# Optimization experiments

Measured on AMD Instinct MI355X. Metric: run time of the kernel, lower is better.

## Reference

```python
import jax, jax.numpy as jnp
import numpy as np

BATCH = 10
HID = 128
OUT = 7
MAX_LEN = 2048


def setup_inputs() -> dict:
    key = jax.random.key(0)
    ks = jax.random.split(key, 10)
    h0 = jax.random.normal(ks[0], (1, BATCH, HID), dtype=jnp.float32)
    c0 = jax.random.normal(ks[1], (1, BATCH, HID), dtype=jnp.float32)
    # target is a sequence of one-hot vectors, shape (MAX_LEN+1, 1, OUT)
    tgt_idx = jax.random.randint(ks[2], (MAX_LEN + 1,), 0, OUT)
    target_onehot = jax.nn.one_hot(tgt_idx, OUT, dtype=jnp.float32)[:, None, :]
    # per-step teacher-forcing coin flips (torch.rand(1) < 0.5 externalized)
    tf_mask = jax.random.bernoulli(ks[3], 0.5, (MAX_LEN,))
    # LSTM parameters, torch gate order [i, f, g, o]; k = 1/sqrt(HID) init scale
    k = 1.0 / np.sqrt(HID)
    W_ih = jax.random.uniform(ks[4], (4 * HID, OUT), minval=-k, maxval=k, dtype=jnp.float32)
    W_hh = jax.random.uniform(ks[5], (4 * HID, HID), minval=-k, maxval=k, dtype=jnp.float32)
    b_ih = jax.random.uniform(ks[6], (4 * HID,), minval=-k, maxval=k, dtype=jnp.float32)
    b_hh = jax.random.uniform(ks[7], (4 * HID,), minval=-k, maxval=k, dtype=jnp.float32)
    W_out = jax.random.uniform(ks[8], (OUT, HID), minval=-k, maxval=k, dtype=jnp.float32)
    b_out = jax.random.uniform(ks[9], (OUT,), minval=-k, maxval=k, dtype=jnp.float32)
    return dict(h0=h0, c0=c0, target_onehot=target_onehot, tf_mask=tf_mask,
                W_ih=W_ih, W_hh=W_hh, b_ih=b_ih, b_hh=b_hh, W_out=W_out, b_out=b_out)


def reference(h0, c0, target_onehot, tf_mask, W_ih, W_hh, b_ih, b_hh, W_out, b_out):
    # initial decoder input: one-hot at last class for all 10 batch items
    x0 = jnp.zeros((BATCH, OUT), jnp.float32).at[:, OUT - 1].set(1.0)
    tgt_next = target_onehot[1:MAX_LEN + 1, 0, :]  # (MAX_LEN, OUT), fed at step i
    bias = b_ih + b_hh

    def step(carry, inp):
        h, c, x = carry            # h,c: (B,HID); x: (B,OUT)
        tf, tgt = inp              # tf: scalar bool; tgt: (OUT,)
        xr = jax.nn.relu(x)
        gates = xr @ W_ih.T + h @ W_hh.T + bias          # (B, 4*HID)
        i_g, f_g, g_g, o_g = jnp.split(gates, 4, axis=-1)
        c2 = jax.nn.sigmoid(f_g) * c + jax.nn.sigmoid(i_g) * jnp.tanh(g_g)
        h2 = jax.nn.sigmoid(o_g) * jnp.tanh(c2)
        logits = h2 @ W_out.T + b_out                    # (B, OUT)
        greedy = jax.nn.one_hot(jnp.argmax(logits, axis=-1), OUT, dtype=jnp.float32)
        nxt = jnp.where(tf, jnp.broadcast_to(tgt, (BATCH, OUT)), greedy)
        return (h2, c2, nxt), logits

    (hT, cT, _), logits = jax.lax.scan(
        step, (h0[0], c0[0], x0), (tf_mask, tgt_next))
    logits = jnp.transpose(logits, (1, 0, 2))            # (B, MAX_LEN, OUT)
    log_probs = jax.nn.log_softmax(logits, axis=-1)
    return log_probs, (hT[None], cT[None])
```

## Files before the change

### kernel.cpp

```cpp
#include <hip/hip_runtime.h>
#include <math.h>

#define BATCH 10
#define HID 128
#define OUT 7
#define MAXLEN 2048
#define NG 512
#define NT 1024
#define RINGD 512
#define OFF_STATE ((size_t)BATCH * MAXLEN * OUT)

typedef float float4v __attribute__((ext_vector_type(4)));

__device__ __forceinline__ float sigm_(float x) { return 1.0f / (1.0f + __expf(-x)); }
__device__ __forceinline__ float tanh_(float x) { return 1.0f - 2.0f / (1.0f + __expf(2.0f * x)); }

__device__ __forceinline__ float grp8_sum(float v) {
    v += __int_as_float(__builtin_amdgcn_update_dpp(0, __float_as_int(v), 0xB1, 0xF, 0xF, true));
    v += __int_as_float(__builtin_amdgcn_update_dpp(0, __float_as_int(v), 0x4E, 0xF, 0xF, true));
    v += __int_as_float(__builtin_amdgcn_update_dpp(0, __float_as_int(v), 0x141, 0xF, 0xF, true));
    return v;
}

__global__
__attribute__((amdgpu_flat_work_group_size(NT, NT), amdgpu_waves_per_eu(4, 4)))
void decoder_rnn_kernel(const float* __restrict__ h0,
                        const float* __restrict__ c0,
                        const float* __restrict__ tonehot,
                        const void*  __restrict__ tf_raw,
                        const float* __restrict__ Wih,
                        const float* __restrict__ Whh,
                        const float* __restrict__ bih,
                        const float* __restrict__ bhh,
                        const float* __restrict__ Wout,
                        const float* __restrict__ bout,
                        float* __restrict__ out)
{
    __shared__ __align__(16) float h_lds[HID];
    __shared__ __align__(16) float gates_lds[NG];
    __shared__ float wih_eff[OUT * NG];
    __shared__ float ring[RINGD][OUT];
    __shared__ unsigned char tgt8[MAXLEN];
    __shared__ unsigned char tf8[MAXLEN];
    __shared__ int tf_byte_mode;

    const int t    = threadIdx.x;
    const int lane = t & 63;
    const int wv   = t >> 6;
    const int ksl  = lane & 7;
    const int grp  = lane >> 3;
    const int b    = blockIdx.x;
    const int gbase = wv * 32 + grp * 4;

    float4v wgt[4][4];
    #pragma unroll
    for (int j = 0; j < 4; j++)
        #pragma unroll
        for (int c = 0; c < 4; c++)
            wgt[j][c] = *(const float4v*)&Whh[(size_t)(gbase + j) * HID + ksl * 16 + c * 4];

    float4v lw[4];
    #pragma unroll
    for (int c = 0; c < 4; c++) { float4v z = {0.f, 0.f, 0.f, 0.f}; lw[c] = z; }
    if (wv < 2 && grp < OUT) {
        #pragma unroll
        for (int c = 0; c < 4; c++)
            lw[c] = *(const float4v*)&Wout[(size_t)grp * HID + ksl * 16 + c * 4];
    }

    float boutr[OUT];
    #pragma unroll
    for (int j = 0; j < OUT; j++) boutr[j] = bout[j];

    for (int idx = t; idx < OUT * NG; idx += NT) {
        int x = idx >> 9, g = idx & (NG - 1);
        wih_eff[idx] = Wih[g * OUT + x] + bih[g] + bhh[g];
    }
    if (t == 0) tf_byte_mode = 0;
    for (int s = t; s < MAXLEN; s += NT) {
        const float* row = tonehot + (size_t)(s + 1) * OUT;
        int idx = 0;
        #pragma unroll
        for (int j = 0; j < OUT; j++) if (row[j] > 0.5f) idx = j;
        tgt8[s] = (unsigned char)idx;
    }
    __syncthreads();
    {
        const unsigned char* tb = (const unsigned char*)tf_raw;
        int mis = 0;
        for (int p = t; p < MAXLEN; p += NT)
            if ((p & 3) && tb[p]) mis = 1;
        if (mis) atomicOr(&tf_byte_mode, 1);
    }
    float c_reg = 0.f, hv = 0.f;
    if (t < HID) {
        hv    = h0[b * HID + t];
        c_reg = c0[b * HID + t];
        h_lds[t] = hv;
    }
    __syncthreads();
    if (tf_byte_mode) {
        const unsigned char* tb = (const unsigned char*)tf_raw;
        for (int s = t; s < MAXLEN; s += NT) tf8[s] = (tb[s] != 0);
    } else {
        const int* ti = (const int*)tf_raw;
        for (int s = t; s < MAXLEN; s += NT) tf8[s] = (ti[s] != 0);
    }
    __syncthreads();

    float* outlp = out + (size_t)b * MAXLEN * OUT;

    for (int s = 0; s < MAXLEN; s++) {
        float4v hc[4];
        #pragma unroll
        for (int c = 0; c < 4; c++)
            hc[c] = *(const float4v*)&h_lds[ksl * 16 + c * 4];

        float a0 = 0.f, a1 = 0.f, a2 = 0.f, a3 = 0.f;
        #pragma unroll
        for (int c = 0; c < 4; c++)
            #pragma unroll
            for (int e = 0; e < 4; e++) {
                const float hval = hc[c][e];
                a0 = fmaf(wgt[0][c][e], hval, a0);
                a1 = fmaf(wgt[1][c][e], hval, a1);
                a2 = fmaf(wgt[2][c][e], hval, a2);
                a3 = fmaf(wgt[3][c][e], hval, a3);
            }
        float al = 0.f;
        if (wv < 2) {
            #pragma unroll
            for (int c = 0; c < 4; c++)
                #pragma unroll
                for (int e = 0; e < 4; e++)
                    al = fmaf(lw[c][e], hc[c][e], al);
            al = grp8_sum(al);
        }
        a0 = grp8_sum(a0);
        a1 = grp8_sum(a1);
        a2 = grp8_sum(a2);
        a3 = grp8_sum(a3);
        if (ksl == 0) {
            float4v g4;
            g4[0] = a0; g4[1] = a1; g4[2] = a2; g4[3] = a3;
            *(float4v*)&gates_lds[gbase] = g4;
        }
        __syncthreads();

        if (t < HID) {
            int xsel = OUT - 1;
            if (s > 0) {
                float lg[OUT];
                lg[0] = __int_as_float(__builtin_amdgcn_readlane(__float_as_int(al),  0)) + boutr[0];
                lg[1] = __int_as_float(__builtin_amdgcn_readlane(__float_as_int(al),  8)) + boutr[1];
                lg[2] = __int_as_float(__builtin_amdgcn_readlane(__float_as_int(al), 16)) + boutr[2];
                lg[3] = __int_as_float(__builtin_amdgcn_readlane(__float_as_int(al), 24)) + boutr[3];
                lg[4] = __int_as_float(__builtin_amdgcn_readlane(__float_as_int(al), 32)) + boutr[4];
                lg[5] = __int_as_float(__builtin_amdgcn_readlane(__float_as_int(al), 40)) + boutr[5];
                lg[6] = __int_as_float(__builtin_amdgcn_readlane(__float_as_int(al), 48)) + boutr[6];
                float bv = lg[0]; int bi = 0;
                #pragma unroll
                for (int j = 1; j < OUT; j++) if (lg[j] > bv) { bv = lg[j]; bi = j; }
                xsel = tf8[s - 1] ? (int)tgt8[s - 1] : bi;
                if (wv == 0 && ksl == 0 && grp < OUT)
                    ring[(s - 1) & (RINGD - 1)][grp] = al;
            }
            const int xo = xsel * NG;
            float ri = gates_lds[t]           + wih_eff[xo + t];
            float rf = gates_lds[HID + t]     + wih_eff[xo + HID + t];
            float rg = gates_lds[2 * HID + t] + wih_eff[xo + 2 * HID + t];
            float ro = gates_lds[3 * HID + t] + wih_eff[xo + 3 * HID + t];
            float cn = sigm_(rf) * c_reg + sigm_(ri) * tanh_(rg);
            c_reg = cn;
            hv = sigm_(ro) * tanh_(cn);
            h_lds[t] = hv;
        } else if (t >= 512 && t < 768 && (s & 255) == 1 && s > 256) {
            const int step = (s - 257) + (t - 512);
            const int slot = step & (RINGD - 1);
            float v[OUT];
            #pragma unroll
            for (int j = 0; j < OUT; j++) v[j] = ring[slot][j] + boutr[j];
            float mx = v[0];
            #pragma unroll
            for (int j = 1; j < OUT; j++) mx = fmaxf(mx, v[j]);
            float sum = 0.f;
            #pragma unroll
            for (int j = 0; j < OUT; j++) sum += __expf(v[j] - mx);
            const float lse = mx + __logf(sum);
            float* dst = outlp + (size_t)step * OUT;
            #pragma unroll
            for (int j = 0; j < OUT; j++) dst[j] = v[j] - lse;
        }
        __syncthreads();
    }

    if (wv < 2) {
        float al = 0.f;
        #pragma unroll
        for (int c = 0; c < 4; c++) {
            float4v hcv = *(const float4v*)&h_lds[ksl * 16 + c * 4];
            #pragma unroll
            for (int e = 0; e < 4; e++) al = fmaf(lw[c][e], hcv[e], al);
        }
        al = grp8_sum(al);
        if (wv == 0 && ksl == 0 && grp < OUT)
            ring[(MAXLEN - 1) & (RINGD - 1)][grp] = al;
    }
    __syncthreads();
    if (t < 256) {
        const int step = (MAXLEN - 256) + t;
        const int slot = step & (RINGD - 1);
        float v[OUT];
        #pragma unroll
        for (int j = 0; j < OUT; j++) v[j] = ring[slot][j] + boutr[j];
        float mx = v[0];
        #pragma unroll
        for (int j = 1; j < OUT; j++) mx = fmaxf(mx, v[j]);
        float sum = 0.f;
        #pragma unroll
        for (int j = 0; j < OUT; j++) sum += __expf(v[j] - mx);
        const float lse = mx + __logf(sum);
        float* dst = outlp + (size_t)step * OUT;
        #pragma unroll
        for (int j = 0; j < OUT; j++) dst[j] = v[j] - lse;
    }
    if (t < HID) {
        out[OFF_STATE + b * HID + t] = hv;
        out[OFF_STATE + BATCH * HID + b * HID + t] = c_reg;
    }
}

extern "C" void kernel_launch(void* const* d_in, const int* in_sizes, int n_in,
                              void* d_out, int out_size, void* d_ws, size_t ws_size,
                              hipStream_t stream) {
    const float* h0    = (const float*)d_in[0];
    const float* c0    = (const float*)d_in[1];
    const float* toh   = (const float*)d_in[2];
    const void*  tfm   = (const void*) d_in[3];
    const float* Wih   = (const float*)d_in[4];
    const float* Whh   = (const float*)d_in[5];
    const float* bih   = (const float*)d_in[6];
    const float* bhh   = (const float*)d_in[7];
    const float* Wout  = (const float*)d_in[8];
    const float* bout  = (const float*)d_in[9];
    float* out = (float*)d_out;

    decoder_rnn_kernel<<<dim3(BATCH), dim3(NT), 0, stream>>>(
        h0, c0, toh, tfm, Wih, Whh, bih, bhh, Wout, bout, out);
}
```

Before: 2.133 ms.

## Halve block size, use packed FMA over 8 gates per thread, move argmax before barrier

The block shrinks from 1024 to 512 threads, so each 8-lane group now computes 8 gate rows instead of 4, with the recurrent weights held in registers as float2 pairs. The dot products use packed 2-wide FMA, and h is read with an interleaved k-layout that avoids LDS bank conflicts. The logit argmax for the next input is computed before the barrier instead of after it, which removes work from the serial section between the two syncs. Register pressure per thread doubles, and the softmax writer threads are remapped to threads 256-511.

```diff
diff --git a/kernel.cpp b/kernel.cpp
--- a/kernel.cpp
+++ b/kernel.cpp
@@ -6,10 +6,11 @@
 #define OUT 7
 #define MAXLEN 2048
 #define NG 512
-#define NT 1024
+#define NT 512
 #define RINGD 512
 #define OFF_STATE ((size_t)BATCH * MAXLEN * OUT)
 
+typedef float float2v __attribute__((ext_vector_type(2)));
 typedef float float4v __attribute__((ext_vector_type(4)));
 
 __device__ __forceinline__ float sigm_(float x) { return 1.0f / (1.0f + __expf(-x)); }
@@ -23,7 +24,7 @@
 }
 
 __global__
-__attribute__((amdgpu_flat_work_group_size(NT, NT), amdgpu_waves_per_eu(4, 4)))
+__attribute__((amdgpu_flat_work_group_size(NT, NT), amdgpu_waves_per_eu(2, 2)))
 void decoder_rnn_kernel(const float* __restrict__ h0,
                         const float* __restrict__ c0,
                         const float* __restrict__ tonehot,
@@ -50,22 +51,26 @@
     const int ksl  = lane & 7;
     const int grp  = lane >> 3;
     const int b    = blockIdx.x;
-    const int gbase = wv * 32 + grp * 4;
-
-    float4v wgt[4][4];
+    const int gbase = wv * 64 + grp * 8;
+
+    float2v wgt2[8][8];
     #pragma unroll
-    for (int j = 0; j < 4; j++)
-        #pragma unroll
-        for (int c = 0; c < 4; c++)
-            wgt[j][c] = *(const float4v*)&Whh[(size_t)(gbase + j) * HID + ksl * 16 + c * 4];
-
-    float4v lw[4];
+    for (int g = 0; g < 8; g++)
+        #pragma unroll
+        for (int p = 0; p < 8; p++) {
+            const int kk = (p >> 1) * 32 + ksl * 4 + (p & 1) * 2;
+            wgt2[g][p] = *(const float2v*)&Whh[(size_t)(gbase + g) * HID + kk];
+        }
+
+    float2v lw2[8];
     #pragma unroll
-    for (int c = 0; c < 4; c++) { float4v z = {0.f, 0.f, 0.f, 0.f}; lw[c] = z; }
+    for (int p = 0; p < 8; p++) { float2v z = {0.f, 0.f}; lw2[p] = z; }
     if (wv < 2 && grp < OUT) {
         #pragma unroll
-        for (int c = 0; c < 4; c++)
-            lw[c] = *(const float4v*)&Wout[(size_t)grp * HID + ksl * 16 + c * 4];
+        for (int p = 0; p < 8; p++) {
+            const int kk = (p >> 1) * 32 + ksl * 4 + (p & 1) * 2;
+            lw2[p] = *(const float2v*)&Wout[(size_t)grp * HID + kk];
+        }
     }
 
     float boutr[OUT];
@@ -114,41 +119,35 @@
         float4v hc[4];
         #pragma unroll
         for (int c = 0; c < 4; c++)
-            hc[c] = *(const float4v*)&h_lds[ksl * 16 + c * 4];
-
-        float a0 = 0.f, a1 = 0.f, a2 = 0.f, a3 = 0.f;
-        #pragma unroll
-        for (int c = 0; c < 4; c++)
-            #pragma unroll
-            for (int e = 0; e < 4; e++) {
-                const float hval = hc[c][e];
-                a0 = fmaf(wgt[0][c][e], hval, a0);
-                a1 = fmaf(wgt[1][c][e], hval, a1);
-                a2 = fmaf(wgt[2][c][e], hval, a2);
-                a3 = fmaf(wgt[3][c][e], hval, a3);
+            hc[c] = *(const float4v*)&h_lds[c * 32 + ksl * 4];
+
+        float2v acc[8];
+        #pragma unroll
+        for (int g = 0; g < 8; g++) { float2v z = {0.f, 0.f}; acc[g] = z; }
+        #pragma unroll
+        for (int p = 0; p < 8; p++) {
+            const float2v hp = (p & 1)
+                ? __builtin_shufflevector(hc[p >> 1], hc[p >> 1], 2, 3)
+                : __builtin_shufflevector(hc[p >> 1], hc[p >> 1], 0, 1);
+            #pragma unroll
+            for (int g = 0; g < 8; g++)
+                acc[g] = __builtin_elementwise_fma(wgt2[g][p], hp, acc[g]);
+        }
+        float a[8];
+        #pragma unroll
+        for (int g = 0; g < 8; g++) a[g] = grp8_sum(acc[g][0] + acc[g][1]);
+
+        int xsel = OUT - 1;
+        if (wv < 2) {
+            float2v accl = {0.f, 0.f};
+            #pragma unroll
+            for (int p = 0; p < 8; p++) {
+                const float2v hp = (p & 1)
+                    ? __builtin_shufflevector(hc[p >> 1], hc[p >> 1], 2, 3)
+                    : __builtin_shufflevector(hc[p >> 1], hc[p >> 1], 0, 1);
+                accl = __builtin_elementwise_fma(lw2[p], hp, accl);
             }
-        float al = 0.f;
-        if (wv < 2) {
-            #pragma unroll
-            for (int c = 0; c < 4; c++)
-                #pragma unroll
-                for (int e = 0; e < 4; e++)
-                    al = fmaf(lw[c][e], hc[c][e], al);
-            al = grp8_sum(al);
-        }
-        a0 = grp8_sum(a0);
-        a1 = grp8_sum(a1);
-        a2 = grp8_sum(a2);
-        a3 = grp8_sum(a3);
-        if (ksl == 0) {
-            float4v g4;
-            g4[0] = a0; g4[1] = a1; g4[2] = a2; g4[3] = a3;
-            *(float4v*)&gates_lds[gbase] = g4;
-        }
-        __syncthreads();
-
-        if (t < HID) {
-            int xsel = OUT - 1;
+            const float al = grp8_sum(accl[0] + accl[1]);
             if (s > 0) {
                 float lg[OUT];
                 lg[0] = __int_as_float(__builtin_amdgcn_readlane(__float_as_int(al),  0)) + boutr[0];
@@ -165,6 +164,17 @@
                 if (wv == 0 && ksl == 0 && grp < OUT)
                     ring[(s - 1) & (RINGD - 1)][grp] = al;
             }
+        }
+        if (ksl == 0) {
+            float4v g4a, g4b;
+            g4a[0] = a[0]; g4a[1] = a[1]; g4a[2] = a[2]; g4a[3] = a[3];
+            g4b[0] = a[4]; g4b[1] = a[5]; g4b[2] = a[6]; g4b[3] = a[7];
+            *(float4v*)&gates_lds[gbase]     = g4a;
+            *(float4v*)&gates_lds[gbase + 4] = g4b;
+        }
+        __syncthreads();
+
+        if (t < HID) {
             const int xo = xsel * NG;
             float ri = gates_lds[t]           + wih_eff[xo + t];
             float rf = gates_lds[HID + t]     + wih_eff[xo + HID + t];
@@ -174,8 +184,8 @@
             c_reg = cn;
             hv = sigm_(ro) * tanh_(cn);
             h_lds[t] = hv;
-        } else if (t >= 512 && t < 768 && (s & 255) == 1 && s > 256) {
-            const int step = (s - 257) + (t - 512);
+        } else if (t >= 256 && (s & 255) == 1 && s > 256) {
+            const int step = (s - 257) + (t - 256);
             const int slot = step & (RINGD - 1);
             float v[OUT];
             #pragma unroll
@@ -195,14 +205,14 @@
     }
 
     if (wv < 2) {
-        float al = 0.f;
-        #pragma unroll
-        for (int c = 0; c < 4; c++) {
-            float4v hcv = *(const float4v*)&h_lds[ksl * 16 + c * 4];
-            #pragma unroll
-            for (int e = 0; e < 4; e++) al = fmaf(lw[c][e], hcv[e], al);
-        }
-        al = grp8_sum(al);
+        float2v accl = {0.f, 0.f};
+        #pragma unroll
+        for (int p = 0; p < 8; p++) {
+            const int kk = (p >> 1) * 32 + ksl * 4 + (p & 1) * 2;
+            const float2v hp = *(const float2v*)&h_lds[kk];
+            accl = __builtin_elementwise_fma(lw2[p], hp, accl);
+        }
+        const float al = grp8_sum(accl[0] + accl[1]);
         if (wv == 0 && ksl == 0 && grp < OUT)
             ring[(MAXLEN - 1) & (RINGD - 1)][grp] = al;
     }
```

Measured after the change: 1.955 ms. 8.3% less time.
